# Performance work log

Measured on AMD Instinct MI355X. Metric: run time of the kernel, lower is better.

## Reference

```python
import jax, jax.numpy as jnp
import numpy as np

N_NODES = 50000
N_EDGES = 1600000
N_FEAT = 256
HDIM = 64
HEADS = 8
N_GRAPHS = 64
NEG_SLOPE = 0.2


def gat_layer(x, src, dst, W, a_src, a_dst, b, heads, out_c, concat):
    # x: [N, F]; W: [F, heads*out_c]; a_src/a_dst: [heads, out_c]; b: bias
    N = x.shape[0]
    h = (x @ W).reshape(N, heads, out_c)              # [N, H, C]
    alpha_s = jnp.sum(h * a_src, axis=-1)             # [N, H]
    alpha_d = jnp.sum(h * a_dst, axis=-1)             # [N, H]
    e = jax.nn.leaky_relu(alpha_s[src] + alpha_d[dst], NEG_SLOPE)  # [E, H]
    # numerically stable segment softmax over incoming edges of each dst node
    m = jax.lax.stop_gradient(jax.ops.segment_max(e, dst, num_segments=N))
    p = jnp.exp(e - m[dst])
    denom = jax.ops.segment_sum(p, dst, num_segments=N)
    alpha = p / denom[dst]                            # [E, H]
    out = jax.ops.segment_sum(h[src] * alpha[:, :, None], dst, num_segments=N)  # [N, H, C]
    out = out.reshape(N, heads * out_c) if concat else out.mean(axis=1)
    return out + b


def setup_inputs() -> dict:
    key = jax.random.key(0)
    ks = jax.random.split(key, 10)
    x = jax.random.normal(ks[0], (N_NODES, N_FEAT), dtype=jnp.float32)
    edge_index = jax.random.randint(ks[1], (2, N_EDGES), 0, N_NODES, dtype=jnp.int64)
    batch = jnp.sort(jax.random.randint(ks[2], (N_NODES,), 0, N_GRAPHS, dtype=jnp.int64))
    c1 = HDIM // HEADS  # 8 channels per head
    s1 = 1.0 / np.sqrt(N_FEAT)
    s2 = 1.0 / np.sqrt(HDIM)
    W1 = jax.random.normal(ks[3], (N_FEAT, HEADS * c1), dtype=jnp.float32) * s1
    a_src1 = jax.random.normal(ks[4], (HEADS, c1), dtype=jnp.float32) * s2
    a_dst1 = jax.random.normal(ks[5], (HEADS, c1), dtype=jnp.float32) * s2
    b1 = jnp.zeros((HEADS * c1,), dtype=jnp.float32)
    W2 = jax.random.normal(ks[6], (HDIM, 1), dtype=jnp.float32) * s2
    a_src2 = jax.random.normal(ks[7], (1, 1), dtype=jnp.float32)
    a_dst2 = jax.random.normal(ks[8], (1, 1), dtype=jnp.float32)
    b2 = jnp.zeros((1,), dtype=jnp.float32)
    return {"x": x, "edge_index": edge_index, "batch": batch,
            "W1": W1, "a_src1": a_src1, "a_dst1": a_dst1, "b1": b1,
            "W2": W2, "a_src2": a_src2, "a_dst2": a_dst2, "b2": b2}


def reference(x, edge_index, batch, W1, a_src1, a_dst1, b1, W2, a_src2, a_dst2, b2):
    N = x.shape[0]
    # PyG GATConv adds self-loops by default
    loops = jnp.arange(N, dtype=edge_index.dtype)
    src = jnp.concatenate([edge_index[0], loops])
    dst = jnp.concatenate([edge_index[1], loops])
    c1 = HDIM // HEADS
    h = gat_layer(x, src, dst, W1, a_src1, a_dst1, b1, HEADS, c1, concat=True)
    h = jax.nn.relu(h)
    # dropout is identity in eval mode (training=False)
    h = gat_layer(h, src, dst, W2, a_src2, a_dst2, b2, 1, 1, concat=False)  # [N, 1]
    # global mean pool over graphs
    counts = jax.ops.segment_sum(jnp.ones((N,), dtype=h.dtype), batch, num_segments=N_GRAPHS)
    sums = jax.ops.segment_sum(h, batch, num_segments=N_GRAPHS)  # [G, 1]
    return sums / jnp.maximum(counts, 1.0)[:, None]
```

## Files before the change

kernel.cpp:

```cpp
#include <hip/hip_runtime.h>
#include <hip/hip_bf16.h>
#include <hip/hip_fp16.h>
#include <math.h>

#define NF 256
#define NO 64
#define NHEAD 8
#define NEG_SLOPE 0.2f
#define BKT 128
#define NBLK 256
#define RCAP 8192

__device__ __forceinline__ float lrelu(float x) { return x > 0.f ? x : NEG_SLOPE * x; }

typedef _Float16 f16x8 __attribute__((ext_vector_type(8)));
typedef float f32x4 __attribute__((ext_vector_type(4)));

__device__ __forceinline__ unsigned f2u(float a, float b) {
    __half2 h = __float22half2_rn(make_float2(a, b));
    return *(unsigned*)&h;
}

__global__ __launch_bounds__(256) void k_front(
    const float* __restrict__ x, const float* __restrict__ W,
    const float* __restrict__ a_src, const float* __restrict__ a_dst,
    __half* __restrict__ h1h, float* __restrict__ as1, float* __restrict__ ad1,
    const int* __restrict__ eidx, unsigned* __restrict__ M,
    float* __restrict__ gacc, int N, int E, int GB, int NB, int CH)
{
    __shared__ unsigned xl2[64][68];
    __shared__ unsigned wl2[64][68];

    if (blockIdx.x >= GB) {
        unsigned* hist = &xl2[0][0];
        for (int i = threadIdx.x; i < NB; i += 256) hist[i] = 0;
        __syncthreads();
        const int blk = blockIdx.x - GB;
        const int lo = blk * CH;
        const int hi = min(lo + CH, E + N);
        for (int i = lo + (int)threadIdx.x; i < hi; i += 256) {
            int d = (i < E) ? eidx[E + i] : (i - E);
            atomicAdd(&hist[d >> 7], 1u);
        }
        __syncthreads();
        for (int b = threadIdx.x; b < NB; b += 256)
            M[(size_t)b * NBLK + blk] = hist[b];
        return;
    }

    if (blockIdx.x == 0) {
        for (int i = threadIdx.x; i < 1024; i += 256) gacc[i] = 0.f;
    }
    const int t   = threadIdx.x;
    const int lw  = t & 63;
    const int wv  = t >> 6;
    const int row0 = blockIdx.x * 64;

    f32x4 acc[4] = {};

    for (int kc = 0; kc < NF; kc += 128) {
        if (kc) __syncthreads();
        {
            const int r = t >> 2, q = t & 3;
            int row = row0 + r; if (row >= N) row = N - 1;
            const float4* xs = (const float4*)(x + (size_t)row * NF + kc + q * 32);
            #pragma unroll
            for (int i = 0; i < 8; ++i) {
                float4 v = xs[i];
                xl2[r][q * 16 + 2 * i]     = f2u(v.x, v.y);
                xl2[r][q * 16 + 2 * i + 1] = f2u(v.z, v.w);
            }
        }
        {
            const int c = t & 63, seg = t >> 6;
            #pragma unroll
            for (int m = 0; m < 16; ++m) {
                int k = kc + seg * 32 + 2 * m;
                float w0 = W[(size_t)k * NO + c];
                float w1 = W[(size_t)(k + 1) * NO + c];
                wl2[c][seg * 16 + m] = f2u(w0, w1);
            }
        }
        __syncthreads();

        const int mrow = 16 * wv + (lw & 15);
        const int fcol = (lw >> 4) * 4;
        #pragma unroll
        for (int ks = 0; ks < 4; ++ks) {
            f16x8 a = *(const f16x8*)&xl2[mrow][ks * 16 + fcol];
            #pragma unroll
            for (int ct = 0; ct < 4; ++ct) {
                f16x8 b = *(const f16x8*)&wl2[16 * ct + (lw & 15)][ks * 16 + fcol];
                acc[ct] = __builtin_amdgcn_mfma_f32_16x16x32_f16(a, b, acc[ct], 0, 0, 0);
            }
        }
    }

    const int colb = lw & 15;
    #pragma unroll
    for (int ct = 0; ct < 4; ++ct) {
        const int col = 16 * ct + colb;
        const float asc = a_src[col];
        const float adc = a_dst[col];
        #pragma unroll
        for (int j = 0; j < 4; ++j) {
            const int rowAbs = row0 + 16 * wv + (lw >> 4) * 4 + j;
            float v = acc[ct][j];
            float vs = v * asc, vd = v * adc;
            vs += __shfl_xor(vs, 1); vs += __shfl_xor(vs, 2); vs += __shfl_xor(vs, 4);
            vd += __shfl_xor(vd, 1); vd += __shfl_xor(vd, 2); vd += __shfl_xor(vd, 4);
            if (rowAbs < N) {
                h1h[(size_t)rowAbs * NO + col] = __float2half(v);
                if ((colb & 7) == 0) {
                    int head = 2 * ct + (colb >> 3);
                    as1[rowAbs * NHEAD + head] = vs;
                    ad1[rowAbs * NHEAD + head] = vd;
                }
            }
        }
    }
}

__global__ __launch_bounds__(1024) void k_scan2(
    unsigned* __restrict__ M, unsigned* __restrict__ Bbase, int NB)
{
    __shared__ unsigned tot[512];
    __shared__ unsigned basel[513];
    const int t = threadIdx.x, lane = t & 63, w = t >> 6;

    for (int b = w; b < NB; b += 16) {
        uint4 v = ((const uint4*)&M[(size_t)b * NBLK])[lane];
        unsigned s = v.x + v.y + v.z + v.w;
        #pragma unroll
        for (int m = 1; m < 64; m <<= 1) s += __shfl_xor(s, m);
        if (lane == 0) tot[b] = s;
    }
    __syncthreads();
    if (t == 0) {
        unsigned r = 0;
        for (int b = 0; b < NB; ++b) { basel[b] = r; r += tot[b]; }
        basel[NB] = r;
    }
    __syncthreads();
    for (int b = t; b <= NB; b += 1024) Bbase[b] = basel[b];
    for (int b = w; b < NB; b += 16) {
        uint4 v = ((const uint4*)&M[(size_t)b * NBLK])[lane];
        unsigned lsum = v.x + v.y + v.z + v.w;
        unsigned p = lsum;
        #pragma unroll
        for (int d = 1; d < 64; d <<= 1) {
            unsigned q = __shfl_up(p, d);
            if (lane >= d) p += q;
        }
        unsigned c0 = basel[b] + p - lsum;
        uint4 o;
        o.x = c0;
        o.y = c0 + v.x;
        o.z = o.y + v.y;
        o.w = o.z + v.z;
        ((uint4*)&M[(size_t)b * NBLK])[lane] = o;
    }
}

__global__ __launch_bounds__(256) void k_bscatter(
    const int* __restrict__ eidx, int E, int N, int NB, int CH,
    const unsigned* __restrict__ M, unsigned* __restrict__ rbuf)
{
    __shared__ unsigned cur[512];
    const int blk = blockIdx.x;
    for (int b = threadIdx.x; b < NB; b += 256)
        cur[b] = M[(size_t)b * NBLK + blk];
    __syncthreads();
    const int lo = blk * CH;
    const int hi = min(lo + CH, E + N);
    for (int i = lo + (int)threadIdx.x; i < hi; i += 256) {
        int s, d;
        if (i < E) { s = eidx[i]; d = eidx[E + i]; }
        else       { s = i - E;   d = i - E; }
        unsigned pos = atomicAdd(&cur[d >> 7], 1u);
        rbuf[pos] = ((unsigned)s << 7) | (unsigned)(d & (BKT - 1));
    }
}

__global__ __launch_bounds__(256) void k_csr(
    const unsigned* __restrict__ Bbase, int N, int NB,
    unsigned* __restrict__ rbuf, unsigned* __restrict__ offs)
{
    __shared__ unsigned recs[RCAP];
    __shared__ unsigned nhist[BKT];
    __shared__ unsigned ncur[BKT];
    __shared__ unsigned wtotS;
    const int b = blockIdx.x;
    const unsigned base = Bbase[b], end = Bbase[b + 1];
    const int cnt = (int)(end - base);
    const int nodes = min(BKT, N - b * BKT);

    for (int i = threadIdx.x; i < BKT; i += 256) nhist[i] = 0;
    __syncthreads();
    for (int i = threadIdx.x; i < cnt; i += 256) {
        unsigned r = rbuf[base + i];
        recs[i] = r;
        atomicAdd(&nhist[r & (BKT - 1)], 1u);
    }
    __syncthreads();
    const int tl = threadIdx.x & 127;
    unsigned v = nhist[tl], p = v;
    #pragma unroll
    for (int d = 1; d < 64; d <<= 1) {
        unsigned q = __shfl_up(p, d);
        if ((tl & 63) >= d) p += q;
    }
    if (threadIdx.x == 63) wtotS = p;
    __syncthreads();
    unsigned excl = base + ((tl >= 64) ? wtotS : 0u) + p - v;
    if (threadIdx.x < 128) {
        ncur[tl] = excl;
        if (tl < nodes) offs[b * BKT + tl] = excl;
    }
    if (b == NB - 1 && threadIdx.x == 0) offs[N] = end;
    __syncthreads();
    for (int i = threadIdx.x; i < cnt; i += 256) {
        unsigned r = recs[i];
        unsigned pos = atomicAdd(&ncur[r & (BKT - 1)], 1u);
        rbuf[pos] = r >> 7;
    }
}

__global__ __launch_bounds__(256) void k_gat1(
    const unsigned* __restrict__ offs, const int* __restrict__ csr,
    const float4* __restrict__ h1q,
    const float* __restrict__ as1, const float* __restrict__ ad1,
    const float* __restrict__ b1, const float* __restrict__ W2,
    float* __restrict__ h2, int N)
{
    const int lane = threadIdx.x & 63;
    const int n = blockIdx.x * (blockDim.x >> 6) + (threadIdx.x >> 6);
    if (n >= N) return;
    const int slot = lane >> 3;
    const int head = lane & 7;
    const unsigned s0 = offs[n];
    const unsigned deg = offs[n + 1] - s0;
    const float ad = ad1[n * NHEAD + head];

    float acc[8] = {};
    float den = 0.f;

    unsigned k = (unsigned)slot;
    for (; k + 24 < deg; k += 32) {
        int sA = csr[s0 + k],      sB = csr[s0 + k + 8];
        int sC = csr[s0 + k + 16], sD = csr[s0 + k + 24];
        float aA = as1[sA * NHEAD + head], aB = as1[sB * NHEAD + head];
        float aC = as1[sC * NHEAD + head], aD = as1[sD * NHEAD + head];
        float4 rA = h1q[(unsigned)sA * 8u + head];
        float4 rB = h1q[(unsigned)sB * 8u + head];
        float4 rC = h1q[(unsigned)sC * 8u + head];
        float4 rD = h1q[(unsigned)sD * 8u + head];
        float pA = __expf(lrelu(aA + ad));
        float pB = __expf(lrelu(aB + ad));
        float pC = __expf(lrelu(aC + ad));
        float pD = __expf(lrelu(aD + ad));
        den += (pA + pB) + (pC + pD);
        const __half2* hA = (const __half2*)&rA;
        const __half2* hB = (const __half2*)&rB;
        const __half2* hC = (const __half2*)&rC;
        const __half2* hD = (const __half2*)&rD;
        #pragma unroll
        for (int j = 0; j < 4; ++j) {
            float2 fA = __half22float2(hA[j]);
            float2 fB = __half22float2(hB[j]);
            float2 fC = __half22float2(hC[j]);
            float2 fD = __half22float2(hD[j]);
            acc[2 * j]     = fmaf(pA, fA.x, acc[2 * j]);
            acc[2 * j + 1] = fmaf(pA, fA.y, acc[2 * j + 1]);
            acc[2 * j]     = fmaf(pB, fB.x, acc[2 * j]);
            acc[2 * j + 1] = fmaf(pB, fB.y, acc[2 * j + 1]);
            acc[2 * j]     = fmaf(pC, fC.x, acc[2 * j]);
            acc[2 * j + 1] = fmaf(pC, fC.y, acc[2 * j + 1]);
            acc[2 * j]     = fmaf(pD, fD.x, acc[2 * j]);
            acc[2 * j + 1] = fmaf(pD, fD.y, acc[2 * j + 1]);
        }
    }
    for (; k + 8 < deg; k += 16) {
        int sA = csr[s0 + k], sB = csr[s0 + k + 8];
        float aA = as1[sA * NHEAD + head], aB = as1[sB * NHEAD + head];
        float4 rA = h1q[(unsigned)sA * 8u + head];
        float4 rB = h1q[(unsigned)sB * 8u + head];
        float pA = __expf(lrelu(aA + ad));
        float pB = __expf(lrelu(aB + ad));
        den += pA + pB;
        const __half2* hA = (const __half2*)&rA;
        const __half2* hB = (const __half2*)&rB;
        #pragma unroll
        for (int j = 0; j < 4; ++j) {
            float2 fA = __half22float2(hA[j]);
            float2 fB = __half22float2(hB[j]);
            acc[2 * j]     = fmaf(pA, fA.x, acc[2 * j]);
            acc[2 * j + 1] = fmaf(pA, fA.y, acc[2 * j + 1]);
            acc[2 * j]     = fmaf(pB, fB.x, acc[2 * j]);
            acc[2 * j + 1] = fmaf(pB, fB.y, acc[2 * j + 1]);
        }
    }
    if (k < deg) {
        int s = csr[s0 + k];
        float a = as1[s * NHEAD + head];
        float4 r = h1q[(unsigned)s * 8u + head];
        float p = __expf(lrelu(a + ad));
        den += p;
        const __half2* hh = (const __half2*)&r;
        #pragma unroll
        for (int j = 0; j < 4; ++j) {
            float2 f = __half22float2(hh[j]);
            acc[2 * j]     = fmaf(p, f.x, acc[2 * j]);
            acc[2 * j + 1] = fmaf(p, f.y, acc[2 * j + 1]);
        }
    }

    #pragma unroll
    for (int r = 0; r < 8; ++r) {
        acc[r] += __shfl_xor(acc[r], 8);
        acc[r] += __shfl_xor(acc[r], 16);
        acc[r] += __shfl_xor(acc[r], 32);
    }
    den += __shfl_xor(den, 8);
    den += __shfl_xor(den, 16);
    den += __shfl_xor(den, 32);

    const float4 b0 = ((const float4*)b1)[head * 2];
    const float4 b1v = ((const float4*)b1)[head * 2 + 1];
    const float4 w0 = ((const float4*)W2)[head * 2];
    const float4 w1v = ((const float4*)W2)[head * 2 + 1];
    const float inv = 1.f / den;
    float tt = 0.f;
    tt += fmaxf(fmaf(acc[0], inv, b0.x), 0.f) * w0.x;
    tt += fmaxf(fmaf(acc[1], inv, b0.y), 0.f) * w0.y;
    tt += fmaxf(fmaf(acc[2], inv, b0.z), 0.f) * w0.z;
    tt += fmaxf(fmaf(acc[3], inv, b0.w), 0.f) * w0.w;
    tt += fmaxf(fmaf(acc[4], inv, b1v.x), 0.f) * w1v.x;
    tt += fmaxf(fmaf(acc[5], inv, b1v.y), 0.f) * w1v.y;
    tt += fmaxf(fmaf(acc[6], inv, b1v.z), 0.f) * w1v.z;
    tt += fmaxf(fmaf(acc[7], inv, b1v.w), 0.f) * w1v.w;
    tt += __shfl_xor(tt, 1);
    tt += __shfl_xor(tt, 2);
    tt += __shfl_xor(tt, 4);
    if (lane == 0) h2[n] = tt;
}

__global__ __launch_bounds__(1024) void k_gat2pool(
    const unsigned* __restrict__ offs, const int* __restrict__ csr,
    const float* __restrict__ h2, const int* __restrict__ batch,
    const float* __restrict__ a_src2, const float* __restrict__ a_dst2,
    const float* __restrict__ b2, float* __restrict__ gacc, int N)
{
    __shared__ float vals[64];
    __shared__ int gid[64];
    const int t = threadIdx.x;
    if (t < 64) gid[t] = -1;
    __syncthreads();

    const int lane = t & 63;
    const int ql = lane & 15;
    const int slot = (t >> 6) * 4 + (lane >> 4);
    const int n = blockIdx.x * 64 + slot;

    if (n < N) {
        const float aS = a_src2[0], aD = a_dst2[0];
        const unsigned s0 = offs[n], s1 = offs[n + 1];
        const float ad = h2[n] * aD;
        float num = 0.f, den = 0.f;
        for (unsigned j = s0 + (unsigned)ql; j < s1; j += 16) {
            float hs = h2[csr[j]];
            float p = __expf(lrelu(hs * aS + ad));
            num = fmaf(p, hs, num);
            den += p;
        }
        #pragma unroll
        for (int msk = 1; msk < 16; msk <<= 1) {
            num += __shfl_xor(num, msk);
            den += __shfl_xor(den, msk);
        }
        if (ql == 0) {
            vals[slot] = num / den + b2[0];
            gid[slot] = batch[n];
        }
    }
    __syncthreads();

    if (t < 64) {
        int g = gid[t];
        float o = (g >= 0) ? vals[t] : 0.f;
        const int g0 = __shfl(g, 0);
        const bool same = (g == g0);
        float s = same ? o : 0.f;
        float c = (same && g >= 0) ? 1.f : 0.f;
        #pragma unroll
        for (int msk = 1; msk < 64; msk <<= 1) {
            s += __shfl_xor(s, msk);
            c += __shfl_xor(c, msk);
        }
        if (t == 0) {
            unsafeAtomicAdd(&gacc[g0 * 16], s);
            unsafeAtomicAdd(&gacc[g0 * 16 + 1], c);
        }
        if (g >= 0 && !same) {
            unsafeAtomicAdd(&gacc[g * 16], o);
            unsafeAtomicAdd(&gacc[g * 16 + 1], 1.0f);
        }
    }
}

__global__ void k_final(const float* __restrict__ gacc,
                        float* __restrict__ out, int G)
{
    int g = blockIdx.x * blockDim.x + threadIdx.x;
    if (g < G) out[g] = gacc[g * 16] / fmaxf(gacc[g * 16 + 1], 1.0f);
}

extern "C" void kernel_launch(void* const* d_in, const int* in_sizes, int n_in,
                              void* d_out, int out_size, void* d_ws, size_t ws_size,
                              hipStream_t stream)
{
    const float* x      = (const float*)d_in[0];
    const int*   eidx   = (const int*)d_in[1];
    const int*   batch  = (const int*)d_in[2];
    const float* W1     = (const float*)d_in[3];
    const float* a_src1 = (const float*)d_in[4];
    const float* a_dst1 = (const float*)d_in[5];
    const float* b1     = (const float*)d_in[6];
    const float* W2     = (const float*)d_in[7];
    const float* a_src2 = (const float*)d_in[8];
    const float* a_dst2 = (const float*)d_in[9];
    const float* b2     = (const float*)d_in[10];

    const int N = in_sizes[0] / NF;
    const int E = in_sizes[1] / 2;
    const int G = out_size;
    const int ETOT = E + N;
    const int NB = (N + BKT - 1) / BKT;
    const int CH = (ETOT + NBLK - 1) / NBLK;
    const int GB = (N + 63) / 64;

    char* w = (char*)d_ws;
    __half*   h1h   = (__half*)(w + 0);
    float*    as1   = (float*)(w + 6400000);
    float*    ad1   = (float*)(w + 8000000);
    float*    h2    = (float*)(w + 9600000);
    unsigned* offs  = (unsigned*)(w + 9800000);
    unsigned* rbuf  = (unsigned*)(w + 10000064);
    unsigned* M     = (unsigned*)(w + 16600064);
    unsigned* Bbase = (unsigned*)(w + 17000448);
    float*    gacc  = (float*)(w + 17002496);

    k_front<<<GB + NBLK, 256, 0, stream>>>(x, W1, a_src1, a_dst1,
                                           h1h, as1, ad1,
                                           eidx, M, gacc, N, E, GB, NB, CH);
    k_scan2<<<1, 1024, 0, stream>>>(M, Bbase, NB);
    k_bscatter<<<NBLK, 256, 0, stream>>>(eidx, E, N, NB, CH, M, rbuf);
    k_csr<<<NB, 256, 0, stream>>>(Bbase, N, NB, rbuf, offs);

    const int* csr = (const int*)rbuf;
    k_gat1<<<(N + 3) / 4, 256, 0, stream>>>(offs, csr, (const float4*)h1h,
                                            as1, ad1, b1, W2, h2, N);
    k_gat2pool<<<(N + 63) / 64, 1024, 0, stream>>>(offs, csr, h2, batch,
                                                   a_src2, a_dst2, b2, gacc, N);
    k_final<<<1, 64, 0, stream>>>(gacc, (float*)d_out, G);
}
```

Baseline: 132.5 us.

## Store source attention logits in fp16 and fold final pooling into last block

The per-node source attention scores used in the layer-1 edge gather are now stored as half precision, which halves the bytes read per gathered edge for that array. The separate final division kernel is removed. The pooling kernel now uses an atomic completion counter so the last block to finish computes the per-graph means. This saves one kernel launch but adds a counter atomic and a threadfence per block, and the fp16 scores lose some precision.

Result: slower. 140.9 us (+6.3%).

```diff
diff --git a/kernel.cpp b/kernel.cpp
--- a/kernel.cpp
+++ b/kernel.cpp
@@ -24,9 +24,10 @@
 __global__ __launch_bounds__(256) void k_front(
     const float* __restrict__ x, const float* __restrict__ W,
     const float* __restrict__ a_src, const float* __restrict__ a_dst,
-    __half* __restrict__ h1h, float* __restrict__ as1, float* __restrict__ ad1,
+    __half* __restrict__ h1h, __half* __restrict__ as1h, float* __restrict__ ad1,
     const int* __restrict__ eidx, unsigned* __restrict__ M,
-    float* __restrict__ gacc, int N, int E, int GB, int NB, int CH)
+    float* __restrict__ gacc, unsigned* __restrict__ dcnt,
+    int N, int E, int GB, int NB, int CH)
 {
     __shared__ unsigned xl2[64][68];
     __shared__ unsigned wl2[64][68];
@@ -50,6 +51,7 @@
 
     if (blockIdx.x == 0) {
         for (int i = threadIdx.x; i < 1024; i += 256) gacc[i] = 0.f;
+        if (threadIdx.x == 0) *dcnt = 0u;
     }
     const int t   = threadIdx.x;
     const int lw  = t & 63;
@@ -113,7 +115,7 @@
                 h1h[(size_t)rowAbs * NO + col] = __float2half(v);
                 if ((colb & 7) == 0) {
                     int head = 2 * ct + (colb >> 3);
-                    as1[rowAbs * NHEAD + head] = vs;
+                    as1h[rowAbs * NHEAD + head] = __float2half(vs);
                     ad1[rowAbs * NHEAD + head] = vd;
                 }
             }
@@ -228,8 +230,8 @@
 
 __global__ __launch_bounds__(256) void k_gat1(
     const unsigned* __restrict__ offs, const int* __restrict__ csr,
-    const float4* __restrict__ h1q,
-    const float* __restrict__ as1, const float* __restrict__ ad1,
+    const float4* __restrict__ h1q, const __half* __restrict__ as1h,
+    const float* __restrict__ ad1,
     const float* __restrict__ b1, const float* __restrict__ W2,
     float* __restrict__ h2, int N)
 {
@@ -249,8 +251,10 @@
     for (; k + 24 < deg; k += 32) {
         int sA = csr[s0 + k],      sB = csr[s0 + k + 8];
         int sC = csr[s0 + k + 16], sD = csr[s0 + k + 24];
-        float aA = as1[sA * NHEAD + head], aB = as1[sB * NHEAD + head];
-        float aC = as1[sC * NHEAD + head], aD = as1[sD * NHEAD + head];
+        float aA = __half2float(as1h[sA * NHEAD + head]);
+        float aB = __half2float(as1h[sB * NHEAD + head]);
+        float aC = __half2float(as1h[sC * NHEAD + head]);
+        float aD = __half2float(as1h[sD * NHEAD + head]);
         float4 rA = h1q[(unsigned)sA * 8u + head];
         float4 rB = h1q[(unsigned)sB * 8u + head];
         float4 rC = h1q[(unsigned)sC * 8u + head];
@@ -282,7 +286,8 @@
     }
     for (; k + 8 < deg; k += 16) {
         int sA = csr[s0 + k], sB = csr[s0 + k + 8];
-        float aA = as1[sA * NHEAD + head], aB = as1[sB * NHEAD + head];
+        float aA = __half2float(as1h[sA * NHEAD + head]);
+        float aB = __half2float(as1h[sB * NHEAD + head]);
         float4 rA = h1q[(unsigned)sA * 8u + head];
         float4 rB = h1q[(unsigned)sB * 8u + head];
         float pA = __expf(lrelu(aA + ad));
@@ -302,7 +307,7 @@
     }
     if (k < deg) {
         int s = csr[s0 + k];
-        float a = as1[s * NHEAD + head];
+        float a = __half2float(as1h[s * NHEAD + head]);
         float4 r = h1q[(unsigned)s * 8u + head];
         float p = __expf(lrelu(a + ad));
         den += p;
@@ -349,10 +354,12 @@
     const unsigned* __restrict__ offs, const int* __restrict__ csr,
     const float* __restrict__ h2, const int* __restrict__ batch,
     const float* __restrict__ a_src2, const float* __restrict__ a_dst2,
-    const float* __restrict__ b2, float* __restrict__ gacc, int N)
+    const float* __restrict__ b2, float* __restrict__ gacc,
+    unsigned* __restrict__ dcnt, float* __restrict__ out, int N, int G)
 {
     __shared__ float vals[64];
     __shared__ int gid[64];
+    __shared__ unsigned lastflag;
     const int t = threadIdx.x;
     if (t < 64) gid[t] = -1;
     __syncthreads();
@@ -406,13 +413,18 @@
             unsafeAtomicAdd(&gacc[g * 16 + 1], 1.0f);
         }
     }
-}
-
-__global__ void k_final(const float* __restrict__ gacc,
-                        float* __restrict__ out, int G)
-{
-    int g = blockIdx.x * blockDim.x + threadIdx.x;
-    if (g < G) out[g] = gacc[g * 16] / fmaxf(gacc[g * 16 + 1], 1.0f);
+    __syncthreads();
+    if (t == 0) {
+        __threadfence();
+        unsigned v = atomicAdd(dcnt, 1u);
+        lastflag = (v == gridDim.x - 1) ? 1u : 0u;
+    }
+    __syncthreads();
+    if (lastflag && t < G) {
+        float s = unsafeAtomicAdd(&gacc[t * 16], 0.0f);
+        float c = unsafeAtomicAdd(&gacc[t * 16 + 1], 0.0f);
+        out[t] = s / fmaxf(c, 1.0f);
+    }
 }
 
 extern "C" void kernel_launch(void* const* d_in, const int* in_sizes, int n_in,
@@ -441,7 +453,7 @@
 
     char* w = (char*)d_ws;
     __half*   h1h   = (__half*)(w + 0);
-    float*    as1   = (float*)(w + 6400000);
+    __half*   as1h  = (__half*)(w + 6400000);
     float*    ad1   = (float*)(w + 8000000);
     float*    h2    = (float*)(w + 9600000);
     unsigned* offs  = (unsigned*)(w + 9800000);
@@ -449,18 +461,19 @@
     unsigned* M     = (unsigned*)(w + 16600064);
     unsigned* Bbase = (unsigned*)(w + 17000448);
     float*    gacc  = (float*)(w + 17002496);
+    unsigned* dcnt  = (unsigned*)(w + 17006592);
 
     k_front<<<GB + NBLK, 256, 0, stream>>>(x, W1, a_src1, a_dst1,
-                                           h1h, as1, ad1,
-                                           eidx, M, gacc, N, E, GB, NB, CH);
+                                           h1h, as1h, ad1,
+                                           eidx, M, gacc, dcnt, N, E, GB, NB, CH);
     k_scan2<<<1, 1024, 0, stream>>>(M, Bbase, NB);
     k_bscatter<<<NBLK, 256, 0, stream>>>(eidx, E, N, NB, CH, M, rbuf);
     k_csr<<<NB, 256, 0, stream>>>(Bbase, N, NB, rbuf, offs);
 
     const int* csr = (const int*)rbuf;
     k_gat1<<<(N + 3) / 4, 256, 0, stream>>>(offs, csr, (const float4*)h1h,
-                                            as1, ad1, b1, W2, h2, N);
+                                            as1h, ad1, b1, W2, h2, N);
     k_gat2pool<<<(N + 63) / 64, 1024, 0, stream>>>(offs, csr, h2, batch,
-                                                   a_src2, a_dst2, b2, gacc, N);
-    k_final<<<1, 64, 0, stream>>>(gacc, (float*)d_out, G);
-}
+                                                   a_src2, a_dst2, b2, gacc,
+                                                   dcnt, (float*)d_out, N, G);
+}
```
